# Kernel optimization log

Measured on AMD Instinct MI355X. Metric: run time of the kernel, lower is better.

## Reference

```python
import jax, jax.numpy as jnp
import numpy as np

N_ATOMS = 20000        # nodes
N_EDGES = 400000       # avg degree 20
C = 4                  # num_pseudo_species channels
F_IN = 128             # ps_input_size
CONV = [64, 64]        # conv_sizes
HID = [64, 32]         # hidden_sizes
OUT = 1                # output_size (energy)
N_STRUCT = 32          # structures in batch
AVG_ATOMS = 20.0       # average_number_of_atoms
NEG_SLOPE = 0.2        # GAT leaky_relu slope


def setup_inputs() -> dict:
    key = jax.random.key(0)
    ks = jax.random.split(key, 16)
    x = jax.random.normal(ks[0], (N_ATOMS, C, F_IN), dtype=jnp.float32)
    edge_index = jax.random.randint(ks[1], (2, N_EDGES), 0, N_ATOMS)
    batch_ids = jnp.sort(jax.random.randint(ks[2], (N_ATOMS,), 0, N_STRUCT))

    def w(k, shape, fan_in):
        return jax.random.normal(k, shape, dtype=jnp.float32) / np.float32(np.sqrt(fan_in))

    return {
        "x": x,
        "edge_index": edge_index,
        "batch_ids": batch_ids,
        "gamma": jnp.ones((F_IN,), jnp.float32),
        "beta": jnp.zeros((F_IN,), jnp.float32),
        # MultiChannelGATConv 1: F_IN -> 64
        "Wc1": w(ks[3], (C, F_IN, CONV[0]), F_IN),
        "asrc1": w(ks[4], (C, CONV[0]), CONV[0]),
        "adst1": w(ks[5], (C, CONV[0]), CONV[0]),
        # MultiChannelGATConv 2: 64 -> 64
        "Wc2": w(ks[6], (C, CONV[0], CONV[1]), CONV[0]),
        "asrc2": w(ks[7], (C, CONV[1]), CONV[1]),
        "adst2": w(ks[8], (C, CONV[1]), CONV[1]),
        # MultiChannelLinear MLP: 64 -> 64 -> 32
        "Wn1": w(ks[9], (C, CONV[1], HID[0]), CONV[1]),
        "Wn2": w(ks[10], (C, HID[0], HID[1]), HID[0]),
        # out_linear: 32 -> 1
        "Wout": w(ks[11], (C, HID[1], OUT), HID[1]),
    }


def _layer_norm(x, gamma, beta):
    mu = jnp.mean(x, axis=-1, keepdims=True)
    var = jnp.mean((x - mu) ** 2, axis=-1, keepdims=True)
    return (x - mu) * jax.lax.rsqrt(var + 1e-5) * gamma + beta


def _gat_conv(x, W, a_src, a_dst, src, dst):
    # per-channel GATConv (single head, no bias): x [N,C,Fin] -> [N,C,Fout]
    h = jnp.einsum('ncf,cfo->nco', x, W)                       # [N,C,Fout]
    e_src = jnp.einsum('nco,co->nc', h, a_src)                 # [N,C]
    e_dst = jnp.einsum('nco,co->nc', h, a_dst)                 # [N,C]
    logit = jax.nn.leaky_relu(e_src[src] + e_dst[dst], NEG_SLOPE)  # [E,C]
    m = jax.ops.segment_max(logit, dst, num_segments=N_ATOMS)      # [N,C]
    ex = jnp.exp(logit - m[dst])                                   # [E,C]
    den = jax.ops.segment_sum(ex, dst, num_segments=N_ATOMS)       # [N,C]
    alpha = ex / (den[dst] + 1e-16)                                # [E,C]
    msg = alpha[:, :, None] * h[src]                               # [E,C,Fout]
    return jax.ops.segment_sum(msg, dst, num_segments=N_ATOMS)     # [N,C,Fout]


def reference(x, edge_index, batch_ids, gamma, beta,
              Wc1, asrc1, adst1, Wc2, asrc2, adst2,
              Wn1, Wn2, Wout):
    src, dst = edge_index[0], edge_index[1]
    h = _layer_norm(x, gamma, beta)
    h = jax.nn.silu(_gat_conv(h, Wc1, asrc1, adst1, src, dst))
    h = jax.nn.silu(_gat_conv(h, Wc2, asrc2, adst2, src, dst))
    h = jax.nn.silu(jnp.einsum('ncf,cfo->nco', h, Wn1))
    h = jax.nn.silu(jnp.einsum('ncf,cfo->nco', h, Wn2))
    h = jnp.einsum('ncf,cfo->nco', h, Wout)                    # [N,C,1]
    feats = jnp.sum(h, axis=1)                                  # sum_over_components -> [N,1]
    energies = jax.ops.segment_sum(feats, batch_ids, num_segments=N_STRUCT)  # [S,1]
    energies = energies / jnp.sqrt(jnp.float32(C))
    energies = energies / jnp.float32(AVG_ATOMS)
    return energies
```

## Files before the change

kernel.cpp:

```cpp
#include <hip/hip_runtime.h>
#include <hip/hip_bf16.h>
#include <hip/hip_fp16.h>

#define N_ATOMS 20000
#define N_EDGES 400000
#define NCH 4
#define F_IN 128
#define S_OUT 32

__device__ __forceinline__ float silu_f(float v) { return v / (1.f + __expf(-v)); }

typedef _Float16 half8v __attribute__((ext_vector_type(8)));
typedef float f32x4v __attribute__((ext_vector_type(4)));

__device__ __forceinline__ half8v ld_frag(const __half* p) {
    union { float4 f; half8v h; } u;
    u.f = *(const float4*)p;
    return u.h;
}

__device__ __forceinline__ int wave_iscan(int v, int l) {
#pragma unroll
    for (int off = 1; off < 64; off <<= 1) {
        int t = __shfl_up(v, off);
        if (l >= off) v += t;
    }
    return v;
}

__global__ void fill_kernel(float* __restrict__ p, int n, float v) {
    int i = blockIdx.x * blockDim.x + threadIdx.x;
    int stride = gridDim.x * blockDim.x;
    for (; i < n; i += stride) p[i] = v;
}

__global__ void hist_kernel(const int* __restrict__ ei, int* __restrict__ cnt, int E) {
    int e = blockIdx.x * 256 + threadIdx.x;
    if (e < E) atomicAdd(&cnt[ei[E + e]], 1);
}

__global__ __launch_bounds__(256) void scan_l1_kernel(const int* __restrict__ cnt,
                                                      int* __restrict__ rowp,
                                                      int* __restrict__ bsum, int n) {
    int i = blockIdx.x * 256 + threadIdx.x;
    int l = threadIdx.x & 63, w = threadIdx.x >> 6;
    int v = (i < n) ? cnt[i] : 0;
    int incl = wave_iscan(v, l);
    __shared__ int wsum[4];
    if (l == 63) wsum[w] = incl;
    __syncthreads();
    int add = 0;
#pragma unroll
    for (int j = 0; j < 4; ++j) add += (j < w) ? wsum[j] : 0;
    if (i < n) rowp[i] = add + incl - v;
    if (threadIdx.x == 255) bsum[blockIdx.x] = add + incl;
}

__global__ __launch_bounds__(256) void scan_l2_kernel(const int* __restrict__ bsum,
                                                      int* __restrict__ boff,
                                                      int* __restrict__ rowp_n, int nb,
                                                      float* __restrict__ out_zero) {
    int i = threadIdx.x;
    if (i < S_OUT) out_zero[i] = 0.f;
    int l = i & 63, w = i >> 6;
    int v = (i < nb) ? bsum[i] : 0;
    int incl = wave_iscan(v, l);
    __shared__ int wsum[4];
    if (l == 63) wsum[w] = incl;
    __syncthreads();
    int add = 0;
#pragma unroll
    for (int j = 0; j < 4; ++j) add += (j < w) ? wsum[j] : 0;
    if (i < nb) boff[i] = add + incl - v;
    if (i == nb - 1) *rowp_n = add + incl;
}

__global__ __launch_bounds__(256) void scan_l3_kernel(int* __restrict__ rowp,
                                                      const int* __restrict__ boff, int n) {
    int i = blockIdx.x * 256 + threadIdx.x;
    if (i < n) rowp[i] += boff[blockIdx.x];
}

__global__ void scatter_kernel(const int* __restrict__ ei, const int* __restrict__ rowp,
                               int* __restrict__ fill, int* __restrict__ csr_src, int E) {
    int e = blockIdx.x * 256 + threadIdx.x;
    if (e < E) {
        int d = ei[E + e];
        int pos = rowp[d] + atomicAdd(&fill[d], 1);
        csr_src[pos] = ei[e];
    }
}

template <int FIN, int IN_STRIDE, bool IN_HALF, bool LN, bool ATT, bool SILU_OUT, bool OUT_HALF>
__global__ __launch_bounds__(256) void proj_kernel(const void* __restrict__ inv,
                                                   const float* __restrict__ gamma,
                                                   const float* __restrict__ beta,
                                                   const float* __restrict__ W,
                                                   const float* __restrict__ a_src,
                                                   const float* __restrict__ a_dst,
                                                   void* __restrict__ outv,
                                                   float* __restrict__ es,
                                                   float* __restrict__ ed) {
    constexpr int OCT = FIN / 8;
    constexpr int OM = OCT - 1;
    constexpr int WSH = FIN + 8;
    __shared__ __half Wt[64 * WSH];
    __shared__ __half inl[64 * WSH];
    const int tid = threadIdx.x;
    const int c = blockIdx.y;
    const int n0 = blockIdx.x * 64;
    const int w = tid >> 6;
    const int l = tid & 63;
    const int col = l & 15;
    const int g = l >> 4;

    const float* __restrict__ Wc = W + c * (FIN * 64);
    for (int i = tid; i < (FIN / 2) * 64; i += 256) {
        int kp = i >> 6, oo = i & 63;
        int k = kp * 2;
        float w0 = Wc[(size_t)k * 64 + oo];
        float w1 = Wc[(size_t)(k + 1) * 64 + oo];
        int pos = ((((k >> 3) ^ (oo >> 2)) & OM) << 3) | (k & 7);
        *(__half2*)(&Wt[oo * WSH + pos]) = __floats2half2_rn(w0, w1);
    }
    if (IN_HALF) {
        const __half* __restrict__ inh = (const __half*)inv;
        for (int i = tid; i < 64 * (FIN / 8); i += 256) {
            int nl = i / (FIN / 8), ch = i % (FIN / 8);
            int node = min(n0 + nl, N_ATOMS - 1);
            *(float4*)(inl + nl * WSH + ch * 8) =
                *(const float4*)(inh + (size_t)node * IN_STRIDE + c * FIN + ch * 8);
        }
    } else {
        const float* __restrict__ inf = (const float*)inv;
        for (int i = tid; i < 64 * (FIN / 8); i += 256) {
            int nl = i / (FIN / 8), ch = i % (FIN / 8);
            int node = min(n0 + nl, N_ATOMS - 1);
            const float* src = inf + (size_t)node * IN_STRIDE + c * FIN + ch * 8;
            float4 a = *(const float4*)src;
            float4 b = *(const float4*)(src + 4);
            float4 st;
            __half2* sp = (__half2*)&st;
            sp[0] = __floats2half2_rn(a.x, a.y);
            sp[1] = __floats2half2_rn(a.z, a.w);
            sp[2] = __floats2half2_rn(b.x, b.y);
            sp[3] = __floats2half2_rn(b.z, b.w);
            *(float4*)(inl + nl * WSH + ch * 8) = st;
        }
    }
    __syncthreads();

    if (LN) {
        float gl0 = gamma[l], gl1 = gamma[l + 64];
        float bl0 = beta[l], bl1 = beta[l + 64];
#pragma unroll
        for (int r = 0; r < 16; ++r) {
            int row = w * 16 + r;
            float v0 = __half2float(inl[row * WSH + l]);
            float v1 = __half2float(inl[row * WSH + l + 64]);
            float s = v0 + v1, sq = v0 * v0 + v1 * v1;
#pragma unroll
            for (int off = 32; off; off >>= 1) {
                s += __shfl_xor(s, off);
                sq += __shfl_xor(sq, off);
            }
            float mu = s * (1.f / 128.f);
            float rs = rsqrtf(sq * (1.f / 128.f) - mu * mu + 1e-5f);
            inl[row * WSH + l]      = __float2half((v0 - mu) * rs * gl0 + bl0);
            inl[row * WSH + l + 64] = __float2half((v1 - mu) * rs * gl1 + bl1);
        }
        __syncthreads();
    }

    f32x4v acc[4];
#pragma unroll
    for (int t = 0; t < 4; ++t) acc[t] = (f32x4v){0.f, 0.f, 0.f, 0.f};

    const __half* arow = inl + (w * 16 + col) * WSH + g * 8;
#pragma unroll
    for (int it = 0; it < FIN / 32; ++it) {
        half8v af = ld_frag(arow + it * 32);
        int J = it * 4 + g;
#pragma unroll
        for (int t = 0; t < 4; ++t) {
            int oo = 16 * t + col;
            half8v bf = ld_frag(Wt + oo * WSH + (((J ^ (oo >> 2)) & OM) << 3));
            acc[t] = __builtin_amdgcn_mfma_f32_16x16x32_f16(af, bf, acc[t], 0, 0, 0);
        }
    }

    float av[4], bv[4];
    if (ATT) {
#pragma unroll
        for (int t = 0; t < 4; ++t) {
            av[t] = a_src[c * 64 + 16 * t + col];
            bv[t] = a_dst[c * 64 + 16 * t + col];
        }
    }
#pragma unroll
    for (int r = 0; r < 4; ++r) {
        int node = n0 + w * 16 + g * 4 + r;
        bool valid = node < N_ATOMS;
        if (valid) {
#pragma unroll
            for (int t = 0; t < 4; ++t) {
                float o = acc[t][r];
                if (SILU_OUT) o = silu_f(o);
                if (OUT_HALF)
                    ((__half*)outv)[(size_t)node * 256 + c * 64 + 16 * t + col] = __float2half(o);
                else
                    ((float*)outv)[(size_t)node * 256 + c * 64 + 16 * t + col] = o;
            }
        }
        if (ATT) {
            float ps = 0.f, pd = 0.f;
#pragma unroll
            for (int t = 0; t < 4; ++t) {
                ps = fmaf(acc[t][r], av[t], ps);
                pd = fmaf(acc[t][r], bv[t], pd);
            }
#pragma unroll
            for (int off = 1; off < 16; off <<= 1) {
                ps += __shfl_xor(ps, off);
                pd += __shfl_xor(pd, off);
            }
            if (col == 0 && valid) { es[node * NCH + c] = ps; ed[node * NCH + c] = pd; }
        }
    }
}

__global__ __launch_bounds__(256) void gat_gather_kernel(const int* __restrict__ rowp,
                                                         const int* __restrict__ csr_src,
                                                         const float* __restrict__ es,
                                                         const float* __restrict__ ed,
                                                         const __half* __restrict__ h,
                                                         __half* __restrict__ out) {
    int l = threadIdx.x & 63;
    int d = blockIdx.x * 4 + (threadIdx.x >> 6);
    int c = l >> 4, q = l & 15;
    int r0 = rowp[d], r1 = rowp[d + 1];
    float edc = ed[d * NCH + c];
    float m = -1e30f, den = 0.f;
    float a0 = 0.f, a1 = 0.f, a2 = 0.f, a3 = 0.f;
    int grp = l & 48;

    for (int base = r0; base < r1; base += 16) {
        int len = min(16, r1 - base);
        float logit = -1e30f;
        int s = 0;
        if (q < len) {
            s = csr_src[base + q];
            float v = es[s * NCH + c] + edc;
            logit = v >= 0.f ? v : 0.2f * v;
        }
        float cm = logit;
#pragma unroll
        for (int off = 8; off; off >>= 1) cm = fmaxf(cm, __shfl_xor(cm, off));
        float nm = fmaxf(m, cm);
        float resc = __expf(m - nm);
        float ex = (q < len) ? __expf(logit - nm) : 0.f;
        float cs = ex;
#pragma unroll
        for (int off = 8; off; off >>= 1) cs += __shfl_xor(cs, off);
        den = den * resc + cs;
        a0 *= resc; a1 *= resc; a2 *= resc; a3 *= resc;
        m = nm;
        int e = 0;
        for (; e + 2 <= len; e += 2) {
            int s0 = __shfl(s, e);
            int s1 = __shfl(s, e + 1);
            float x0 = __shfl(ex, grp | e);
            float x1 = __shfl(ex, grp | (e + 1));
            float2 hv0 = *(const float2*)(h + (size_t)s0 * 256 + l * 4);
            float2 hv1 = *(const float2*)(h + (size_t)s1 * 256 + l * 4);
            __half2* hp0 = (__half2*)&hv0;
            __half2* hp1 = (__half2*)&hv1;
            float2 f00 = __half22float2(hp0[0]), f01 = __half22float2(hp0[1]);
            float2 f10 = __half22float2(hp1[0]), f11 = __half22float2(hp1[1]);
            a0 = fmaf(x0, f00.x, fmaf(x1, f10.x, a0));
            a1 = fmaf(x0, f00.y, fmaf(x1, f10.y, a1));
            a2 = fmaf(x0, f01.x, fmaf(x1, f11.x, a2));
            a3 = fmaf(x0, f01.y, fmaf(x1, f11.y, a3));
        }
        for (; e < len; ++e) {
            int se = __shfl(s, e);
            float xe = __shfl(ex, grp | e);
            float2 hv = *(const float2*)(h + (size_t)se * 256 + l * 4);
            __half2* hp = (__half2*)&hv;
            float2 f0 = __half22float2(hp[0]), f1 = __half22float2(hp[1]);
            a0 = fmaf(xe, f0.x, a0);
            a1 = fmaf(xe, f0.y, a1);
            a2 = fmaf(xe, f1.x, a2);
            a3 = fmaf(xe, f1.y, a3);
        }
    }
    float inv = 1.f / (den + 1e-16f);
    float2 st;
    __half2* sp = (__half2*)&st;
    sp[0] = __floats2half2_rn(silu_f(a0 * inv), silu_f(a1 * inv));
    sp[1] = __floats2half2_rn(silu_f(a2 * inv), silu_f(a3 * inv));
    *(float2*)(out + (size_t)d * 256 + l * 4) = st;
}

__global__ __launch_bounds__(256) void mlp23_kernel(const float* __restrict__ t1g,
                                                    const float* __restrict__ W2,
                                                    const float* __restrict__ W3,
                                                    const int* __restrict__ bat,
                                                    float* __restrict__ out) {
    __shared__ float W2t[NCH * 32 * 68];
    __shared__ float t1l[32 * 260];
    __shared__ float w3l[NCH * 32];
    const int tid = threadIdx.x;
    const int n0 = blockIdx.x * 32;
    const int np = tid >> 3;
    const int o8 = tid & 7;

    for (int i = tid; i < NCH * 2048; i += 256) {
        int cc = i >> 11, rem = i & 2047;
        int k = rem >> 5, o2 = rem & 31;
        W2t[cc * (32 * 68) + o2 * 68 + ((((k >> 2) ^ (o2 >> 2)) & 15) << 2 | (k & 3))] = W2[i];
    }
    for (int i = tid; i < 32 * 256; i += 256) {
        int nl = i >> 8, j = i & 255;
        t1l[nl * 260 + j] = t1g[(size_t)(n0 + nl) * 256 + j];
    }
    if (tid < NCH * 32) w3l[tid] = W3[tid];
    __syncthreads();

    float y = 0.f;
#pragma unroll
    for (int c = 0; c < NCH; ++c) {
        const float* ip = t1l + np * 260 + c * 64;
        const float* wp = W2t + c * (32 * 68) + (o8 * 4) * 68;
        float a0 = 0.f, a1 = 0.f, a2 = 0.f, a3 = 0.f;
#pragma unroll 4
        for (int kq = 0; kq < 16; ++kq) {
            int skq = ((kq ^ o8) & 15) << 2;
            float4 v = *(const float4*)(ip + (kq << 2));
            float4 w0 = *(const float4*)(wp + skq);
            float4 w1 = *(const float4*)(wp + 68 + skq);
            float4 w2 = *(const float4*)(wp + 136 + skq);
            float4 w3 = *(const float4*)(wp + 204 + skq);
            a0 = fmaf(v.x, w0.x, fmaf(v.y, w0.y, fmaf(v.z, w0.z, fmaf(v.w, w0.w, a0))));
            a1 = fmaf(v.x, w1.x, fmaf(v.y, w1.y, fmaf(v.z, w1.z, fmaf(v.w, w1.w, a1))));
            a2 = fmaf(v.x, w2.x, fmaf(v.y, w2.y, fmaf(v.z, w2.z, fmaf(v.w, w2.w, a2))));
            a3 = fmaf(v.x, w3.x, fmaf(v.y, w3.y, fmaf(v.z, w3.z, fmaf(v.w, w3.w, a3))));
        }
        float4 w34 = *(const float4*)(w3l + c * 32 + o8 * 4);
        y += silu_f(a0) * w34.x + silu_f(a1) * w34.y + silu_f(a2) * w34.z + silu_f(a3) * w34.w;
    }
#pragma unroll
    for (int off = 1; off < 8; off <<= 1) y += __shfl_xor(y, off);

    int l = tid & 63;
    int w = tid >> 6;
    float yn = __shfl(y, (l & 7) * 8);
    bool active = l < 8;
    int node = n0 + w * 8 + (l & 7);
    float val = yn * 0.025f;
    int b = bat[node];
    unsigned long long rem = __ballot(active);
    while (rem) {
        int lead = (int)__ffsll(rem) - 1;
        int bl = __shfl(b, lead);
        bool mine = active && (b == bl);
        float t = mine ? val : 0.f;
#pragma unroll
        for (int off = 1; off < 8; off <<= 1) t += __shfl_xor(t, off);
        if (l == lead) atomicAdd(out + bl, t);
        rem &= ~__ballot(mine);
    }
}

extern "C" void kernel_launch(void* const* d_in, const int* in_sizes, int n_in,
                              void* d_out, int out_size, void* d_ws, size_t ws_size,
                              hipStream_t stream) {
    const float* x     = (const float*)d_in[0];
    const int*   ei    = (const int*)d_in[1];
    const int*   bat   = (const int*)d_in[2];
    const float* gamma = (const float*)d_in[3];
    const float* beta  = (const float*)d_in[4];
    const float* Wc1   = (const float*)d_in[5];
    const float* as1   = (const float*)d_in[6];
    const float* ad1   = (const float*)d_in[7];
    const float* Wc2   = (const float*)d_in[8];
    const float* as2   = (const float*)d_in[9];
    const float* ad2   = (const float*)d_in[10];
    const float* Wn1   = (const float*)d_in[11];
    const float* Wn2   = (const float*)d_in[12];
    const float* Wout  = (const float*)d_in[13];
    float* out = (float*)d_out;

    float* A    = (float*)d_ws;
    float* B    = A + 10240000;
    float* es   = B + 5120000;
    float* ed   = es + 80000;
    int* rowp   = (int*)(ed + 80000);
    int* cnt    = rowp + 20004;
    int* fillc  = cnt + 20000;
    int* csr    = fillc + 20000;
    int* bsum   = csr + 400000;
    int* boff   = bsum + 128;
    __half* C1h = (__half*)A;
    __half* C2h = (__half*)(A + 2560000);
    __half* Bh  = (__half*)B;
    float* t1g  = B;

    dim3 blk(256);
    const int NB = (N_ATOMS + 255) / 256;
    const int NT64 = (N_ATOMS + 63) / 64;
    const int NT = N_ATOMS / 32;

    fill_kernel<<<80, blk, 0, stream>>>((float*)cnt, 40000, 0.f);
    hist_kernel<<<(N_EDGES + 255) / 256, blk, 0, stream>>>(ei, cnt, N_EDGES);
    scan_l1_kernel<<<NB, blk, 0, stream>>>(cnt, rowp, bsum, N_ATOMS);
    scan_l2_kernel<<<1, blk, 0, stream>>>(bsum, boff, rowp + N_ATOMS, NB, out);
    scan_l3_kernel<<<NB, blk, 0, stream>>>(rowp, boff, N_ATOMS);
    scatter_kernel<<<(N_EDGES + 255) / 256, blk, 0, stream>>>(ei, rowp, fillc, csr, N_EDGES);

    proj_kernel<128, NCH * F_IN, false, true, true, false, true>
        <<<dim3(NT64, NCH), blk, 0, stream>>>(x, gamma, beta, Wc1, as1, ad1, Bh, es, ed);
    gat_gather_kernel<<<N_ATOMS / 4, blk, 0, stream>>>(rowp, csr, es, ed, Bh, C1h);

    proj_kernel<64, 256, true, false, true, false, true>
        <<<dim3(NT64, NCH), blk, 0, stream>>>(C1h, gamma, beta, Wc2, as2, ad2, Bh, es, ed);
    gat_gather_kernel<<<N_ATOMS / 4, blk, 0, stream>>>(rowp, csr, es, ed, Bh, C2h);

    proj_kernel<64, 256, true, false, false, true, false>
        <<<dim3(NT64, NCH), blk, 0, stream>>>(C2h, gamma, beta, Wn1, as1, ad1, t1g, es, ed);
    mlp23_kernel<<<NT, blk, 0, stream>>>(t1g, Wn2, Wout, bat, out);
}
```

Baseline: 210.5 us.

## Fuse MLP layer 1 into tail kernel with fp16 MFMA for all layers

Replaces the separate Wn1 projection kernel and the fp32 mlp23 kernel with one fused kernel. It computes the first MLP layer, the second layer and the output dot per 64-node tile using fp16 MFMA 16x16x32 instructions, keeping intermediates in LDS. This removes one launch and the fp32 t1 round-trip through global memory (20000x256 floats written then read). In exchange, weights are converted to fp16 in every block, which lowers the second layer's precision, and W1 is reloaded once per channel with extra barriers.

```diff
diff --git a/kernel.cpp b/kernel.cpp
--- a/kernel.cpp
+++ b/kernel.cpp
@@ -302,73 +302,124 @@
     *(float2*)(out + (size_t)d * 256 + l * 4) = st;
 }
 
-__global__ __launch_bounds__(256) void mlp23_kernel(const float* __restrict__ t1g,
-                                                    const float* __restrict__ W2,
-                                                    const float* __restrict__ W3,
-                                                    const int* __restrict__ bat,
-                                                    float* __restrict__ out) {
-    __shared__ float W2t[NCH * 32 * 68];
-    __shared__ float t1l[32 * 260];
+__global__ __launch_bounds__(256) void mlp_fused_kernel(const __half* __restrict__ in,
+                                                        const float* __restrict__ W1,
+                                                        const float* __restrict__ W2,
+                                                        const float* __restrict__ W3,
+                                                        const int* __restrict__ bat,
+                                                        float* __restrict__ out) {
+    constexpr int WSH = 72;
+    __shared__ __half W1t[64 * WSH];
+    __shared__ __half inl[64 * WSH];
+    __shared__ __half t1l[64 * WSH];
+    __shared__ __half W2t[NCH][32 * WSH];
     __shared__ float w3l[NCH * 32];
+    __shared__ float ynode[64];
     const int tid = threadIdx.x;
-    const int n0 = blockIdx.x * 32;
-    const int np = tid >> 3;
-    const int o8 = tid & 7;
-
-    for (int i = tid; i < NCH * 2048; i += 256) {
-        int cc = i >> 11, rem = i & 2047;
-        int k = rem >> 5, o2 = rem & 31;
-        W2t[cc * (32 * 68) + o2 * 68 + ((((k >> 2) ^ (o2 >> 2)) & 15) << 2 | (k & 3))] = W2[i];
-    }
-    for (int i = tid; i < 32 * 256; i += 256) {
-        int nl = i >> 8, j = i & 255;
-        t1l[nl * 260 + j] = t1g[(size_t)(n0 + nl) * 256 + j];
+    const int n0 = blockIdx.x * 64;
+    const int w = tid >> 6;
+    const int l = tid & 63;
+    const int col = l & 15;
+    const int g = l >> 4;
+
+    for (int i = tid; i < NCH * 32 * 32; i += 256) {
+        int cc = i >> 10, rem = i & 1023;
+        int kp = rem >> 5, o2 = rem & 31;
+        int k = kp * 2;
+        float a = W2[cc * 2048 + k * 32 + o2];
+        float b = W2[cc * 2048 + (k + 1) * 32 + o2];
+        int pos = ((((k >> 3) ^ (o2 >> 2)) & 7) << 3) | (k & 7);
+        *(__half2*)(&W2t[cc][o2 * WSH + pos]) = __floats2half2_rn(a, b);
     }
     if (tid < NCH * 32) w3l[tid] = W3[tid];
+
+    float yacc[4] = {0.f, 0.f, 0.f, 0.f};
+
+    for (int c = 0; c < NCH; ++c) {
+        __syncthreads();
+        for (int i = tid; i < 32 * 64; i += 256) {
+            int kp = i >> 6, oo = i & 63;
+            int k = kp * 2;
+            float a = W1[c * 4096 + k * 64 + oo];
+            float b = W1[c * 4096 + (k + 1) * 64 + oo];
+            int pos = ((((k >> 3) ^ (oo >> 2)) & 7) << 3) | (k & 7);
+            *(__half2*)(&W1t[oo * WSH + pos]) = __floats2half2_rn(a, b);
+        }
+        for (int i = tid; i < 64 * 8; i += 256) {
+            int nl = i >> 3, ch = i & 7;
+            int node = min(n0 + nl, N_ATOMS - 1);
+            *(float4*)(inl + nl * WSH + ch * 8) =
+                *(const float4*)(in + (size_t)node * 256 + c * 64 + ch * 8);
+        }
+        __syncthreads();
+
+        f32x4v acc[4];
+#pragma unroll
+        for (int t = 0; t < 4; ++t) acc[t] = (f32x4v){0.f, 0.f, 0.f, 0.f};
+        const __half* arow = inl + (w * 16 + col) * WSH + g * 8;
+#pragma unroll
+        for (int it = 0; it < 2; ++it) {
+            half8v af = ld_frag(arow + it * 32);
+            int J = it * 4 + g;
+#pragma unroll
+            for (int t = 0; t < 4; ++t) {
+                int oo = 16 * t + col;
+                half8v bf = ld_frag(W1t + oo * WSH + (((J ^ (oo >> 2)) & 7) << 3));
+                acc[t] = __builtin_amdgcn_mfma_f32_16x16x32_f16(af, bf, acc[t], 0, 0, 0);
+            }
+        }
+#pragma unroll
+        for (int t = 0; t < 4; ++t)
+#pragma unroll
+            for (int r = 0; r < 4; ++r)
+                t1l[(w * 16 + g * 4 + r) * WSH + 16 * t + col] = __float2half(silu_f(acc[t][r]));
+
+        f32x4v acc2[2];
+        acc2[0] = (f32x4v){0.f, 0.f, 0.f, 0.f};
+        acc2[1] = (f32x4v){0.f, 0.f, 0.f, 0.f};
+        const __half* arow2 = t1l + (w * 16 + col) * WSH + g * 8;
+#pragma unroll
+        for (int it = 0; it < 2; ++it) {
+            half8v af = ld_frag(arow2 + it * 32);
+            int J = it * 4 + g;
+#pragma unroll
+            for (int t = 0; t < 2; ++t) {
+                int o2 = 16 * t + col;
+                half8v bf = ld_frag(&W2t[c][o2 * WSH + (((J ^ (o2 >> 2)) & 7) << 3)]);
+                acc2[t] = __builtin_amdgcn_mfma_f32_16x16x32_f16(af, bf, acc2[t], 0, 0, 0);
+            }
+        }
+        float w3a = w3l[c * 32 + col], w3b = w3l[c * 32 + 16 + col];
+#pragma unroll
+        for (int r = 0; r < 4; ++r) {
+            float p = silu_f(acc2[0][r]) * w3a + silu_f(acc2[1][r]) * w3b;
+#pragma unroll
+            for (int off = 1; off < 16; off <<= 1) p += __shfl_xor(p, off);
+            yacc[r] += p;
+        }
+    }
+
+    if (col == 0) {
+#pragma unroll
+        for (int r = 0; r < 4; ++r) ynode[w * 16 + g * 4 + r] = yacc[r];
+    }
     __syncthreads();
-
-    float y = 0.f;
-#pragma unroll
-    for (int c = 0; c < NCH; ++c) {
-        const float* ip = t1l + np * 260 + c * 64;
-        const float* wp = W2t + c * (32 * 68) + (o8 * 4) * 68;
-        float a0 = 0.f, a1 = 0.f, a2 = 0.f, a3 = 0.f;
-#pragma unroll 4
-        for (int kq = 0; kq < 16; ++kq) {
-            int skq = ((kq ^ o8) & 15) << 2;
-            float4 v = *(const float4*)(ip + (kq << 2));
-            float4 w0 = *(const float4*)(wp + skq);
-            float4 w1 = *(const float4*)(wp + 68 + skq);
-            float4 w2 = *(const float4*)(wp + 136 + skq);
-            float4 w3 = *(const float4*)(wp + 204 + skq);
-            a0 = fmaf(v.x, w0.x, fmaf(v.y, w0.y, fmaf(v.z, w0.z, fmaf(v.w, w0.w, a0))));
-            a1 = fmaf(v.x, w1.x, fmaf(v.y, w1.y, fmaf(v.z, w1.z, fmaf(v.w, w1.w, a1))));
-            a2 = fmaf(v.x, w2.x, fmaf(v.y, w2.y, fmaf(v.z, w2.z, fmaf(v.w, w2.w, a2))));
-            a3 = fmaf(v.x, w3.x, fmaf(v.y, w3.y, fmaf(v.z, w3.z, fmaf(v.w, w3.w, a3))));
-        }
-        float4 w34 = *(const float4*)(w3l + c * 32 + o8 * 4);
-        y += silu_f(a0) * w34.x + silu_f(a1) * w34.y + silu_f(a2) * w34.z + silu_f(a3) * w34.w;
-    }
-#pragma unroll
-    for (int off = 1; off < 8; off <<= 1) y += __shfl_xor(y, off);
-
-    int l = tid & 63;
-    int w = tid >> 6;
-    float yn = __shfl(y, (l & 7) * 8);
-    bool active = l < 8;
-    int node = n0 + w * 8 + (l & 7);
-    float val = yn * 0.025f;
-    int b = bat[node];
-    unsigned long long rem = __ballot(active);
-    while (rem) {
-        int lead = (int)__ffsll(rem) - 1;
-        int bl = __shfl(b, lead);
-        bool mine = active && (b == bl);
-        float t = mine ? val : 0.f;
-#pragma unroll
-        for (int off = 1; off < 8; off <<= 1) t += __shfl_xor(t, off);
-        if (l == lead) atomicAdd(out + bl, t);
-        rem &= ~__ballot(mine);
+    if (tid < 64) {
+        int node = n0 + tid;
+        bool act = node < N_ATOMS;
+        float val = act ? ynode[tid] * 0.025f : 0.f;
+        int b = act ? bat[min(node, N_ATOMS - 1)] : 0;
+        unsigned long long rem = __ballot(act);
+        while (rem) {
+            int lead = (int)__ffsll(rem) - 1;
+            int bl = __shfl(b, lead);
+            bool mine = act && (b == bl);
+            float t = mine ? val : 0.f;
+#pragma unroll
+            for (int off = 32; off; off >>= 1) t += __shfl_xor(t, off);
+            if (tid == lead) atomicAdd(out + bl, t);
+            rem &= ~__ballot(mine);
+        }
     }
 }
 
@@ -404,12 +455,10 @@
     __half* C1h = (__half*)A;
     __half* C2h = (__half*)(A + 2560000);
     __half* Bh  = (__half*)B;
-    float* t1g  = B;
 
     dim3 blk(256);
     const int NB = (N_ATOMS + 255) / 256;
     const int NT64 = (N_ATOMS + 63) / 64;
-    const int NT = N_ATOMS / 32;
 
     fill_kernel<<<80, blk, 0, stream>>>((float*)cnt, 40000, 0.f);
     hist_kernel<<<(N_EDGES + 255) / 256, blk, 0, stream>>>(ei, cnt, N_EDGES);
@@ -426,7 +475,5 @@
         <<<dim3(NT64, NCH), blk, 0, stream>>>(C1h, gamma, beta, Wc2, as2, ad2, Bh, es, ed);
     gat_gather_kernel<<<N_ATOMS / 4, blk, 0, stream>>>(rowp, csr, es, ed, Bh, C2h);
 
-    proj_kernel<64, 256, true, false, false, true, false>
-        <<<dim3(NT64, NCH), blk, 0, stream>>>(C2h, gamma, beta, Wn1, as1, ad1, t1g, es, ed);
-    mlp23_kernel<<<NT, blk, 0, stream>>>(t1g, Wn2, Wout, bat, out);
-}
+    mlp_fused_kernel<<<NT64, blk, 0, stream>>>(C2h, Wn1, Wn2, Wout, bat, out);
+}
```

Measured after the change: 186.2 us. 11.5% less time.
